# Optimization experiments

Hardware: AMD Instinct MI355X
Metric: run time of the kernel (lower is better)

The kernel has to match this reference:

```python
import jax, jax.numpy as jnp
import numpy as np

DIM = 128
HEADS = 4
KV_RANK = 64
Q_RANK = 32
ROPE = DIM // 2   # 64
NOPE = DIM // 2   # 64
VDIM = DIM // 2   # 64
B, H, W = 2, 64, 64
EPS = 1e-5


def _conv1x1(x, w, b):
    # x: [B,C,H,W], w: [O,C], b: [O]
    return jnp.einsum('bchw,oc->bohw', x, w) + b[None, :, None, None]


def _gn1(x, g, b):
    # GroupNorm with 1 group: normalize over (C,H,W) per sample
    mu = jnp.mean(x, axis=(1, 2, 3), keepdims=True)
    var = jnp.mean((x - mu) ** 2, axis=(1, 2, 3), keepdims=True)
    return (x - mu) / jnp.sqrt(var + EPS) * g[None, :, None, None] + b[None, :, None, None]


def _freqs(h, w):
    # Replicates RotaryPositionalEncoding: pe[...,0::4]=sin_h, 1::4=cos_h, 2::4=sin_w, 3::4=cos_w
    n = ROPE // 4
    inv = 1.0 / (10000.0 ** (jnp.arange(n, dtype=jnp.float32) / n))
    ah = jnp.arange(h, dtype=jnp.float32)[:, None] * inv  # [h,n]
    aw = jnp.arange(w, dtype=jnp.float32)[:, None] * inv  # [w,n]
    fh = jnp.stack([jnp.sin(ah), jnp.cos(ah)], -1)  # [h,n,2] -> (real=sin_h, imag=cos_h)
    fw = jnp.stack([jnp.sin(aw), jnp.cos(aw)], -1)  # [w,n,2]
    fh_b = jnp.broadcast_to(fh[:, None], (h, w, n, 2))
    fw_b = jnp.broadcast_to(fw[None, :], (h, w, n, 2))
    # interleave pairs: pair 2m -> fh[m], pair 2m+1 -> fw[m]
    pe = jnp.stack([fh_b, fw_b], axis=3).reshape(h * w, ROPE // 2, 2)
    return pe  # [S, ROPE//2, 2]


def _rope(x, f):
    # x: [..., S, ROPE]; f: [S, ROPE//2, 2]
    xp = x.reshape(x.shape[:-1] + (ROPE // 2, 2))
    fr, fi = f[..., 0], f[..., 1]  # [S, ROPE//2] broadcast over leading dims
    rr = xp[..., 0] * fr - xp[..., 1] * fi
    ri = xp[..., 0] * fi + xp[..., 1] * fr
    return jnp.stack([rr, ri], -1).reshape(x.shape)


def setup_inputs() -> dict:
    key = jax.random.key(0)
    ks = jax.random.split(key, 8)
    s = 0.02
    inp = {
        'x': jax.random.normal(ks[0], (B, DIM, H, W), dtype=jnp.float32),
        'q1_w': jax.random.normal(ks[1], (Q_RANK, DIM), dtype=jnp.float32) * s,
        'q1_b': jnp.zeros((Q_RANK,), jnp.float32),
        'q_gn_g': jnp.ones((Q_RANK,), jnp.float32),
        'q_gn_b': jnp.zeros((Q_RANK,), jnp.float32),
        'q2_w': jax.random.normal(ks[2], (HEADS * (NOPE + ROPE), Q_RANK), dtype=jnp.float32) * s,
        'q2_b': jnp.zeros((HEADS * (NOPE + ROPE),), jnp.float32),
        'kv1_w': jax.random.normal(ks[3], (KV_RANK + ROPE, DIM), dtype=jnp.float32) * s,
        'kv1_b': jnp.zeros((KV_RANK + ROPE,), jnp.float32),
        'kv_gn_g': jnp.ones((KV_RANK + ROPE,), jnp.float32),
        'kv_gn_b': jnp.zeros((KV_RANK + ROPE,), jnp.float32),
        'kvn_g': jnp.ones((KV_RANK,), jnp.float32),
        'kvn_b': jnp.zeros((KV_RANK,), jnp.float32),
        'kvup_w': jax.random.normal(ks[4], (HEADS * (NOPE + VDIM), KV_RANK), dtype=jnp.float32) * s,
        'kvup_b': jnp.zeros((HEADS * (NOPE + VDIM),), jnp.float32),
        'out_w': jax.random.normal(ks[5], (DIM, HEADS * VDIM), dtype=jnp.float32) * s,
        'out_b': jnp.zeros((DIM,), jnp.float32),
    }
    return inp


def reference(x, q1_w, q1_b, q_gn_g, q_gn_b, q2_w, q2_b, kv1_w, kv1_b, kv_gn_g, kv_gn_b, kvn_g, kvn_b, kvup_w, kvup_b, out_w, out_b):
    b, c, h, w = x.shape
    s = h * w
    f = _freqs(h, w)  # [S, ROPE//2, 2]

    # Q path: low-rank down -> GN -> up
    q = _conv1x1(_gn1(_conv1x1(x, q1_w, q1_b), q_gn_g, q_gn_b), q2_w, q2_b)
    q = q.reshape(b, HEADS, NOPE + ROPE, s).transpose(0, 1, 3, 2)  # [B,H,S,D]
    q_nope, q_rope = q[..., :NOPE], q[..., NOPE:]
    q = jnp.concatenate([q_nope, _rope(q_rope, f)], axis=-1)

    # KV path: joint down-proj, split rope-k and compressed kv
    kv = _gn1(_conv1x1(x, kv1_w, kv1_b), kv_gn_g, kv_gn_b)  # [B, ROPE+KV_RANK, H, W]
    k_rope_c, kv_c = kv[:, :ROPE], kv[:, ROPE:]
    kv_u = _conv1x1(_gn1(kv_c, kvn_g, kvn_b), kvup_w, kvup_b)
    kv_u = kv_u.reshape(b, HEADS, NOPE + VDIM, s).transpose(0, 1, 3, 2)
    k_nope, v = kv_u[..., :NOPE], kv_u[..., NOPE:]

    k_rope = _rope(k_rope_c.reshape(b, ROPE, s).transpose(0, 2, 1)[:, None], f)  # [B,1,S,ROPE]
    k = jnp.concatenate([k_nope, jnp.broadcast_to(k_rope, (b, HEADS, s, ROPE))], axis=-1)

    scale = (NOPE + ROPE) ** -0.5
    attn = jax.nn.softmax(jnp.einsum('bhqd,bhkd->bhqk', q, k) * scale, axis=-1)
    o = jnp.einsum('bhqk,bhkd->bhqd', attn, v)  # [B,H,S,VDIM]
    o = o.transpose(0, 1, 3, 2).reshape(b, HEADS * VDIM, h, w)
    return _conv1x1(o, out_w, out_b) + x
```

## Files before the change

### kernel.cpp

```cpp
#include <hip/hip_runtime.h>

typedef unsigned short ushort_t;
typedef unsigned int uint_t;
typedef __attribute__((ext_vector_type(8))) short s16x8;
typedef __attribute__((ext_vector_type(4))) short s16x4;
typedef __attribute__((ext_vector_type(4))) float f32x4;
typedef __attribute__((ext_vector_type(16))) float f32x16;

#define S_TOT 4096
#define QSCALE 0.08838834764831845f
#define LOG2E 1.4426950408889634f
#define QSL (QSCALE * LOG2E)
#define L2_10000_D16 0.8304820237218406f

__device__ __forceinline__ ushort_t f2b(float f) {
  uint_t u = __float_as_uint(f);
  uint_t r = (u + 0x7FFFu + ((u >> 16) & 1u)) >> 16;
  return (ushort_t)r;
}

__device__ __forceinline__ float b2f(ushort_t u) {
  return __uint_as_float((uint_t)u << 16);
}

__device__ __forceinline__ uint_t cvt_pk_bf16(float lo, float hi) {
  uint_t r;
  asm("v_cvt_pk_bf16_f32 %0, %1, %2" : "=v"(r) : "v"(lo), "v"(hi));
  return r;
}

__device__ __forceinline__ void gload16(const void* g, void* l) {
  __builtin_amdgcn_global_load_lds(
      (const __attribute__((address_space(1))) unsigned int*)g,
      (__attribute__((address_space(3))) unsigned int*)l, 16, 0, 0);
}

__device__ __forceinline__ void rope_pair_t(float& x0, float& x1, int p, int hi, int wi,
                                            float scale, const float2* __restrict__ tab) {
  int j = p >> 1;
  int src = (p & 1) ? wi : hi;
  float2 sc = tab[src * 16 + j];
  float r0 = (x0 * sc.x - x1 * sc.y) * scale;
  float r1 = (x0 * sc.y + x1 * sc.x) * scale;
  x0 = r0; x1 = r1;
}

__global__ __launch_bounds__(256) void k_conv1(
    const float* __restrict__ x, const float* __restrict__ q1_w, const float* __restrict__ q1_b,
    const float* __restrict__ kv1_w, const float* __restrict__ kv1_b,
    float* __restrict__ y_q, float* __restrict__ y_kv,
    const float* __restrict__ q2_w, const float* __restrict__ q2_b,
    const float* __restrict__ kvup_w, const float* __restrict__ kvup_b,
    const float* __restrict__ out_w, const float* __restrict__ out_b,
    ushort_t* __restrict__ wq2, ushort_t* __restrict__ wout,
    float* __restrict__ q2b2, float* __restrict__ outb2) {
  if (blockIdx.x >= 256) {
    int E = (blockIdx.x - 256) * 256 + threadIdx.x;
    if (E < 16384) {
      int oc = E >> 5, r = E & 31;
      int h = oc >> 7, d = oc & 127;
      float val;
      if (d < 64) {
        val = 0.f;
        for (int dd = 0; dd < 64; dd++)
          val += kvup_w[(h * 128 + dd) * 64 + d] * q2_w[(size_t)(h * 128 + dd) * 32 + r];
      } else {
        val = q2_w[(size_t)oc * 32 + r];
      }
      wq2[(size_t)oc * 32 + r] = f2b(val);
    } else if (E < 49152) {
      int e = E - 16384;
      int c = e >> 8, col = e & 255;
      int h = col >> 6, l = col & 63;
      float val = 0.f;
      for (int vd = 0; vd < 64; vd++)
        val += out_w[(size_t)c * 256 + h * 64 + vd] * kvup_w[(h * 128 + 64 + vd) * 64 + l];
      wout[(size_t)c * 256 + col] = f2b(val);
    } else if (E < 49664) {
      int oc = E - 49152;
      int h = oc >> 7, d = oc & 127;
      float val;
      if (d < 64) {
        val = 0.f;
        for (int dd = 0; dd < 64; dd++)
          val += kvup_w[(h * 128 + dd) * 64 + d] * q2_b[h * 128 + dd];
      } else val = q2_b[oc];
      q2b2[oc] = val;
    } else if (E < 49792) {
      int c = E - 49664;
      float val = out_b[c];
      for (int j = 0; j < 256; j++) {
        int h = j >> 6, vd = j & 63;
        val += out_w[(size_t)c * 256 + j] * kvup_b[h * 128 + 64 + vd];
      }
      outb2[c] = val;
    }
    return;
  }
  const int id = blockIdx.x;
  const int b = id >> 7, blk = id & 127, st = blk * 32;
  const int t = threadIdx.x, wid = t >> 6;
  const int l15 = t & 15, lg = (t >> 4) & 3;
  __shared__ __align__(16) ushort_t Xt[32][128];
  {
    const int si = t & 31, g = t >> 5;
#pragma unroll
    for (int half = 0; half < 2; half++) {
      ushort_t pk[8];
#pragma unroll
      for (int j = 0; j < 8; j++) {
        int c = g * 16 + half * 8 + j;
        pk[j] = f2b(x[(size_t)(b * 128 + c) * S_TOT + st + si]);
      }
      *(s16x8*)((char*)&Xt[si][0] + ((g * 32 + half * 16) ^ ((si & 15) << 4))) = *(s16x8*)pk;
    }
  }
  __syncthreads();
#pragma unroll
  for (int k5 = 0; k5 < 5; k5++) {
    const int tt = wid * 5 + k5;
    const int rt = tt >> 1, ct = tt & 1;
    const int oc0 = rt * 16;
    f32x4 acc;
#pragma unroll
    for (int r = 0; r < 4; r++) {
      int oc = oc0 + lg * 4 + r;
      acc[r] = (oc < 32) ? q1_b[oc] : kv1_b[oc - 32];
    }
    const int wrow = oc0 + l15;
    const float4* wr4 = (wrow < 32) ? ((const float4*)q1_w) + (size_t)wrow * 32
                                    : ((const float4*)kv1_w) + (size_t)(wrow - 32) * 32;
    const int xrow = ct * 16 + l15;
    const int xswz = (xrow & 15) << 4;
#pragma unroll
    for (int kk = 0; kk < 4; kk++) {
      float4 wa = wr4[kk * 8 + lg * 2];
      float4 wb = wr4[kk * 8 + lg * 2 + 1];
      ushort_t wp[8];
      wp[0] = f2b(wa.x); wp[1] = f2b(wa.y); wp[2] = f2b(wa.z); wp[3] = f2b(wa.w);
      wp[4] = f2b(wb.x); wp[5] = f2b(wb.y); wp[6] = f2b(wb.z); wp[7] = f2b(wb.w);
      s16x8 wf = *(s16x8*)wp;
      s16x8 xf = *(const s16x8*)((const char*)&Xt[xrow][0] + ((kk * 64 + lg * 16) ^ xswz));
      acc = __builtin_amdgcn_mfma_f32_16x16x32_bf16(wf, xf, acc, 0, 0, 0);
    }
    const int sp = st + ct * 16 + l15;
#pragma unroll
    for (int r = 0; r < 4; r++) {
      int oc = oc0 + lg * 4 + r;
      if (oc < 32) y_q[(size_t)(b * 32 + oc) * S_TOT + sp] = acc[r];
      else         y_kv[(size_t)(b * 128 + oc - 32) * S_TOT + sp] = acc[r];
    }
  }
}

__global__ __launch_bounds__(256) void k_red(
    const float* __restrict__ y_q, const float* __restrict__ y_kv,
    double* __restrict__ SQ) {
  const int pair = blockIdx.x, tid = threadIdx.x;
  const int lane = tid & 63, wid = tid >> 6;
  const int b = pair / 160, c = pair % 160;
  const float* row = (c < 32) ? y_q + ((size_t)(b * 32 + c) << 12)
                              : y_kv + ((size_t)(b * 128 + c - 32) << 12);
  const float4* r4 = (const float4*)row;
  double s = 0, q = 0;
#pragma unroll
  for (int j = 0; j < 4; j++) {
    float4 v = r4[tid * 4 + j];
    s += (double)v.x + (double)v.y + (double)v.z + (double)v.w;
    q += (double)v.x * v.x + (double)v.y * v.y + (double)v.z * v.z + (double)v.w * v.w;
  }
#pragma unroll
  for (int o = 1; o < 64; o <<= 1) { s += __shfl_xor(s, o, 64); q += __shfl_xor(q, o, 64); }
  __shared__ double red[4][2];
  if (lane == 0) { red[wid][0] = s; red[wid][1] = q; }
  __syncthreads();
  if (tid == 0) {
    SQ[pair * 2]     = red[0][0] + red[1][0] + red[2][0] + red[3][0];
    SQ[pair * 2 + 1] = red[0][1] + red[1][1] + red[2][1] + red[3][1];
  }
}

__global__ __launch_bounds__(512) void k_stats(
    const double* __restrict__ SQ,
    const float* __restrict__ qg, const float* __restrict__ qb,
    const float* __restrict__ kvg, const float* __restrict__ kvb,
    const float* __restrict__ kng, const float* __restrict__ knb,
    float* __restrict__ coef, float2* __restrict__ tab) {
  __shared__ double Sh[2][160], Qh[2][160];
  const int tid = threadIdx.x;
  for (int i = tid; i < 1024; i += 512) {
    int src = i >> 4, j = i & 15;
    float inv = exp2f(-(float)j * L2_10000_D16);
    float ang = (float)src * inv;
    tab[i] = make_float2(sinf(ang), cosf(ang));
  }
  if (tid < 320) {
    int b = tid / 160, c = tid % 160;
    Sh[b][c] = SQ[tid * 2]; Qh[b][c] = SQ[tid * 2 + 1];
  }
  __syncthreads();
  if (tid < 2) {
    int b = tid;
    float* cf = coef + b * 320;
    const double NS = 4096.0;
    double muq = 0, m2q = 0;
    for (int c = 0; c < 32; c++) { muq += Sh[b][c]; m2q += Qh[b][c]; }
    muq /= (32.0 * NS); m2q /= (32.0 * NS);
    double rstdq = 1.0 / sqrt(m2q - muq * muq + 1e-5);
    for (int c = 0; c < 32; c++) {
      double A = rstdq * (double)qg[c];
      cf[c] = (float)A; cf[32 + c] = (float)((double)qb[c] - muq * A);
    }
    double mukv = 0, m2kv = 0;
    for (int c = 0; c < 128; c++) { mukv += Sh[b][32 + c]; m2kv += Qh[b][32 + c]; }
    mukv /= (128.0 * NS); m2kv /= (128.0 * NS);
    double rstdkv = 1.0 / sqrt(m2kv - mukv * mukv + 1e-5);
    for (int c = 0; c < 64; c++) {
      double A = rstdkv * (double)kvg[c];
      cf[64 + c] = (float)A; cf[128 + c] = (float)((double)kvb[c] - mukv * A);
    }
    double mu2 = 0, m22 = 0;
    for (int c2 = 0; c2 < 64; c2++) {
      int c = 64 + c2;
      double a = rstdkv * (double)kvg[c], bb = (double)kvb[c] - mukv * a;
      double Ec = Sh[b][32 + c] / NS, M2c = Qh[b][32 + c] / NS;
      mu2 += a * Ec + bb;
      m22 += a * a * M2c + 2.0 * a * bb * Ec + bb * bb;
    }
    mu2 /= 64.0; m22 /= 64.0;
    double rstd2 = 1.0 / sqrt(m22 - mu2 * mu2 + 1e-5);
    for (int c2 = 0; c2 < 64; c2++) {
      int c = 64 + c2;
      double a = rstdkv * (double)kvg[c], bb = (double)kvb[c] - mukv * a;
      cf[192 + c2] = (float)(a * rstd2 * (double)kng[c2]);
      cf[256 + c2] = (float)((bb - mu2) * rstd2 * (double)kng[c2] + (double)knb[c2]);
    }
  }
}

__device__ __forceinline__ void gq_body(
    int id, ushort_t* smem,
    const float* __restrict__ y_q, const float* __restrict__ coef,
    const ushort_t* __restrict__ wq2, const float* __restrict__ q2b2,
    const float2* __restrict__ tab, ushort_t* __restrict__ Q) {
  const int h = id & 3, st = (id >> 2) & 63, b = id >> 8;
  const int t = threadIdx.x, si = t & 63, wid = t >> 6;
  const int l15 = t & 15, lg = (t >> 4) & 3;
  const float* cf = coef + b * 320;
  ushort_t* Xt = smem;
  ushort_t* sQ = smem + 4096;
  {
    ushort_t pk[8];
#pragma unroll
    for (int j = 0; j < 8; j++) {
      int c = wid * 8 + j;
      float v = y_q[(size_t)(b * 32 + c) * S_TOT + st * 64 + si];
      pk[j] = f2b(v * cf[c] + cf[32 + c]);
    }
    *(s16x8*)((char*)(Xt + si * 64) + ((wid * 16) ^ ((si & 7) << 4))) = *(s16x8*)pk;
  }
  __syncthreads();
  const int d0w = wid * 32;
  f32x4 acc[2][4];
#pragma unroll
  for (int db = 0; db < 2; db++) {
    f32x4 bv;
#pragma unroll
    for (int r = 0; r < 4; r++) bv[r] = q2b2[h * 128 + d0w + db * 16 + lg * 4 + r];
#pragma unroll
    for (int sb = 0; sb < 4; sb++) acc[db][sb] = bv;
  }
  s16x8 wf[2];
#pragma unroll
  for (int db = 0; db < 2; db++)
    wf[db] = *(const s16x8*)(wq2 + (size_t)(h * 128 + d0w + db * 16 + l15) * 32 + lg * 8);
  const int xsw = (lg * 16) ^ ((l15 & 7) << 4);
#pragma unroll
  for (int sb = 0; sb < 4; sb++) {
    s16x8 xf = *(const s16x8*)((const char*)(Xt + (sb * 16 + l15) * 64) + xsw);
#pragma unroll
    for (int db = 0; db < 2; db++)
      acc[db][sb] = __builtin_amdgcn_mfma_f32_16x16x32_bf16(wf[db], xf, acc[db][sb], 0, 0, 0);
  }
  if (wid >= 2) {
#pragma unroll
    for (int db = 0; db < 2; db++)
#pragma unroll
      for (int sb = 0; sb < 4; sb++) {
        int sp = st * 64 + sb * 16 + l15, hi = sp >> 6, wi = sp & 63;
        int dg = d0w + db * 16 + lg * 4;
#pragma unroll
        for (int pr = 0; pr < 2; pr++) {
          float v0 = acc[db][sb][pr * 2], v1 = acc[db][sb][pr * 2 + 1];
          int p = (dg + pr * 2 - 64) >> 1;
          rope_pair_t(v0, v1, p, hi, wi, QSL, tab);
          acc[db][sb][pr * 2] = v0; acc[db][sb][pr * 2 + 1] = v1;
        }
      }
  } else {
#pragma unroll
    for (int db = 0; db < 2; db++)
#pragma unroll
      for (int sb = 0; sb < 4; sb++)
#pragma unroll
        for (int r = 0; r < 4; r++) acc[db][sb][r] *= QSL;
  }
#pragma unroll
  for (int db = 0; db < 2; db++)
#pragma unroll
    for (int sb = 0; sb < 4; sb++) {
      ushort_t pk[4];
#pragma unroll
      for (int r = 0; r < 4; r++) pk[r] = f2b(acc[db][sb][r]);
      int srow = sb * 16 + l15;
      *(s16x4*)((char*)(sQ + srow * 128) + (((d0w + db * 16 + lg * 4) * 2) ^ ((srow & 7) << 4))) =
          *(s16x4*)pk;
    }
  __syncthreads();
  ushort_t* qrow = Q + ((size_t)(b * 4 + h) * S_TOT + st * 64 + si) * 128 + wid * 32;
#pragma unroll
  for (int j = 0; j < 4; j++) {
    s16x8 v = *(const s16x8*)((const char*)(sQ + si * 128) + ((wid * 64 + j * 16) ^ ((si & 7) << 4)));
    *(s16x8*)(qrow + j * 8) = v;
  }
}

__device__ __forceinline__ void lat_body(
    int blk, const float* __restrict__ y_kv, const float* __restrict__ coef,
    const float2* __restrict__ tab, ushort_t* __restrict__ C, ushort_t* __restrict__ VT) {
  const int b = blk >> 6, st = (blk & 63) * 64;
  const int t = threadIdx.x, si = t & 63, g = t >> 6;
  const float* cf = coef + b * 320;
  const int sp = st + si;
  if (g < 2) {
    const int c0 = g * 32;
    float v[32];
#pragma unroll
    for (int j = 0; j < 32; j++) {
      int c = c0 + j;
      v[j] = y_kv[(size_t)(b * 128 + c) * S_TOT + sp] * cf[64 + c] + cf[128 + c];
    }
    const int hi = sp >> 6, wi = sp & 63;
#pragma unroll
    for (int k = 0; k < 16; k++)
      rope_pair_t(v[2 * k], v[2 * k + 1], (c0 >> 1) + k, hi, wi, 1.0f, tab);
    ushort_t pk[32];
#pragma unroll
    for (int j = 0; j < 32; j++) pk[j] = f2b(v[j]);
    ushort_t* crow = C + (size_t)(b * S_TOT + sp) * 128 + 64 + c0;
#pragma unroll
    for (int j4 = 0; j4 < 4; j4++) *(s16x8*)(crow + j4 * 8) = *(s16x8*)(pk + j4 * 8);
  } else {
    const int c0 = (g - 2) * 32;
    ushort_t pk[32];
#pragma unroll
    for (int j = 0; j < 32; j++) {
      int c2 = c0 + j;
      float v = y_kv[(size_t)(b * 128 + 64 + c2) * S_TOT + sp] * cf[192 + c2] + cf[256 + c2];
      ushort_t u = f2b(v);
      pk[j] = u;
      VT[(size_t)(b * 64 + c2) * S_TOT + sp] = u;
    }
    ushort_t* crow = C + (size_t)(b * S_TOT + sp) * 128 + c0;
#pragma unroll
    for (int j4 = 0; j4 < 4; j4++) *(s16x8*)(crow + j4 * 8) = *(s16x8*)(pk + j4 * 8);
  }
}

__global__ __launch_bounds__(256) void k_build(
    const float* __restrict__ y_q, const float* __restrict__ y_kv,
    const float* __restrict__ coef,
    const ushort_t* __restrict__ wq2, const float* __restrict__ q2b2,
    const float2* __restrict__ tab,
    ushort_t* __restrict__ Q, ushort_t* __restrict__ C, ushort_t* __restrict__ VT) {
  __shared__ __align__(16) ushort_t smem[12288];
  if (blockIdx.x < 512) gq_body(blockIdx.x, smem, y_q, coef, wq2, q2b2, tab, Q);
  else                  lat_body(blockIdx.x - 512, y_kv, coef, tab, C, VT);
}

__global__ __launch_bounds__(256, 2) void k_attn(
    const ushort_t* __restrict__ Q, const ushort_t* __restrict__ C,
    const ushort_t* __restrict__ VT, ushort_t* __restrict__ Opart,
    float* __restrict__ lvec) {
  const int bid = blockIdx.x;
  const int bh = bid & 7;
  const int rest = bid >> 3;
  const int half = rest >> 5, qblk = rest & 31;
  const int kv0 = half * 2048;
  const int tid = threadIdx.x;
  const int wid = tid >> 6, lane = tid & 63;
  const int l31 = lane & 31, hi = lane >> 5;
  const int qbase = qblk * 128 + wid * 32;
  const int b4 = bh >> 2;
  const ushort_t* Qp = Q + (size_t)bh * S_TOT * 128;
  const ushort_t* Kp = C + (size_t)b4 * S_TOT * 128;
  const ushort_t* Vp = VT + (size_t)b4 * 64 * S_TOT;

  __shared__ __align__(16) ushort_t K_lds[3][64][128];
  __shared__ __align__(16) ushort_t V_lds[3][64][64];

  s16x8 qf[8];
#pragma unroll
  for (int c = 0; c < 8; c++)
    qf[c] = *(const s16x8*)(Qp + (size_t)(qbase + l31) * 128 + c * 16 + hi * 8);

  f32x16 o0, o1;
#pragma unroll
  for (int r = 0; r < 16; r++) { o0[r] = 0.f; o1[r] = 0.f; }
  float l_s = 0.f;

  const int krow_l = tid >> 4;
  const int kcolb = (tid & 15) * 16;
  const int vrow_l = tid >> 3;
  const int vcolb = (tid & 7) * 16;

#define STAGE(kvb, bufi)                                                          \
  {                                                                               \
    _Pragma("unroll")                                                             \
    for (int i = 0; i < 4; i++) {                                                 \
      int row = i * 16 + krow_l;                                                  \
      int colb = kcolb ^ ((row & 15) << 4);                                       \
      gload16((const char*)(Kp + (size_t)((kvb) + row) * 128) + colb,             \
              (void*)&K_lds[bufi][i * 16 + wid * 4][0]);                          \
    }                                                                             \
    _Pragma("unroll")                                                             \
    for (int i = 0; i < 2; i++) {                                                 \
      int vd = i * 32 + vrow_l;                                                   \
      int colb = vcolb ^ ((vd & 7) << 4);                                         \
      gload16((const char*)(Vp + (size_t)vd * S_TOT + (kvb)) + colb,              \
              (void*)&V_lds[bufi][i * 32 + wid * 8][0]);                          \
    }                                                                             \
  }

  STAGE(kv0, 0);
  STAGE(kv0 + 64, 1);

  const int kswz = (l31 & 15) << 4;
  const int vswz = (l31 & 7) << 4;
#pragma unroll 1
  for (int t = 0; t < 32; t++) {
    const int buf = t % 3;
    if (t < 31) {
      asm volatile("s_waitcnt vmcnt(6)" ::: "memory");
    } else {
      asm volatile("s_waitcnt vmcnt(0)" ::: "memory");
    }
    __builtin_amdgcn_sched_barrier(0);
    __builtin_amdgcn_s_barrier();
    __builtin_amdgcn_sched_barrier(0);
    if (t < 30) STAGE(kv0 + (t + 2) * 64, (t + 2) % 3);
    f32x16 sc0, sc1;
#pragma unroll
    for (int r = 0; r < 16; r++) { sc0[r] = 0.f; sc1[r] = 0.f; }
    __builtin_amdgcn_s_setprio(1);
#pragma unroll
    for (int c = 0; c < 8; c++) {
      const int off = (c * 32 + hi * 16) ^ kswz;
      s16x8 k0 = *(const s16x8*)((const char*)&K_lds[buf][l31][0] + off);
      s16x8 k1 = *(const s16x8*)((const char*)&K_lds[buf][32 + l31][0] + off);
      sc0 = __builtin_amdgcn_mfma_f32_32x32x16_bf16(k0, qf[c], sc0, 0, 0, 0);
      sc1 = __builtin_amdgcn_mfma_f32_32x32x16_bf16(k1, qf[c], sc1, 0, 0, 0);
    }
    __builtin_amdgcn_s_setprio(0);
    float rs = 0.f;
#pragma unroll
    for (int r = 0; r < 16; r++) {
      float p0 = exp2f(sc0[r]);
      float p1 = exp2f(sc1[r]);
      sc0[r] = p0; sc1[r] = p1;
      rs += p0 + p1;
    }
    l_s += rs;
    __builtin_amdgcn_s_setprio(1);
#pragma unroll
    for (int c = 0; c < 4; c++) {
      const f32x16 P = (c < 2) ? sc0 : sc1;
      const int rA = 8 * (c & 1);
      uint_t a0 = cvt_pk_bf16(P[rA + 0], P[rA + 1]);
      uint_t a1 = cvt_pk_bf16(P[rA + 2], P[rA + 3]);
      uint_t b0 = cvt_pk_bf16(P[rA + 4], P[rA + 5]);
      uint_t b1 = cvt_pk_bf16(P[rA + 6], P[rA + 7]);
      asm volatile("v_permlane32_swap_b32 %0, %1" : "+v"(a0), "+v"(b0));
      asm volatile("v_permlane32_swap_b32 %0, %1" : "+v"(a1), "+v"(b1));
      union { uint_t u[4]; s16x8 v; } pf;
      pf.u[0] = a0; pf.u[1] = a1;
      pf.u[2] = b0; pf.u[3] = b1;
      const int voff = (c * 32 + hi * 16) ^ vswz;
      s16x8 v0 = *(const s16x8*)((const char*)&V_lds[buf][l31][0] + voff);
      s16x8 v1 = *(const s16x8*)((const char*)&V_lds[buf][32 + l31][0] + voff);
      o0 = __builtin_amdgcn_mfma_f32_32x32x16_bf16(v0, pf.v, o0, 0, 0, 0);
      o1 = __builtin_amdgcn_mfma_f32_32x32x16_bf16(v1, pf.v, o1, 0, 0, 0);
    }
    __builtin_amdgcn_s_setprio(0);
  }
#undef STAGE
  l_s += __shfl_xor(l_s, 32, 64);
  if (lane < 32)
    lvec[((size_t)(half * 8 + bh) << 12) + qbase + l31] = l_s;
  char* sO = (char*)&K_lds[0][0][0];
#pragma unroll
  for (int vt = 0; vt < 2; vt++) {
#pragma unroll
    for (int r = 0; r < 16; r += 2) {
      float v0 = (vt ? o1[r] : o0[r]);
      float v1 = (vt ? o1[r + 1] : o0[r + 1]);
      uint_t u = cvt_pk_bf16(v0, v1);
      int vd = vt * 32 + (r & 3) + 8 * (r >> 2) + 4 * hi;
      *(uint_t*)(sO + (wid * 32 + l31) * 128 + ((vd * 2) ^ ((l31 & 7) << 4))) = u;
    }
  }
  __syncthreads();
  {
    const int r = tid >> 1, hf = tid & 1;
    const int w = r >> 5, ql = r & 31;
    ushort_t* orow = Opart + ((size_t)(half * 8 + bh) * S_TOT + qblk * 128 + r) * 64 + hf * 32;
#pragma unroll
    for (int j = 0; j < 4; j++) {
      s16x8 v = *(const s16x8*)(sO + (w * 32 + ql) * 128 + ((hf * 64 + j * 16) ^ ((ql & 7) << 4)));
      *(s16x8*)(orow + j * 8) = v;
    }
  }
}

__global__ __launch_bounds__(256) void k_oc(
    const ushort_t* __restrict__ Opart, const float* __restrict__ lvec,
    const ushort_t* __restrict__ wout, const float* __restrict__ outb2,
    const float* __restrict__ x, float* __restrict__ out) {
  const int id = blockIdx.x;
  const int cch = id & 1, st32 = (id >> 1) & 127, b = id >> 8;
  const int t = threadIdx.x, wid = t >> 6;
  const int l15 = t & 15, lg = (t >> 4) & 3;
  __shared__ __align__(16) ushort_t Xt[32][256];
  {
    const int s = t & 31, grp = t >> 5;
    const int h = grp >> 1, vd0 = (grp & 1) * 32;
    const int sp = st32 * 32 + s;
    const float l0 = lvec[((size_t)(b * 4 + h) << 12) + sp];
    const float l1 = lvec[((size_t)(8 + b * 4 + h) << 12) + sp];
    const float w = 1.f / (l0 + l1);
    const ushort_t* oa = Opart + ((size_t)(b * 4 + h) * S_TOT + sp) * 64 + vd0;
    const ushort_t* obp = oa + (size_t)8 * S_TOT * 64;
#pragma unroll
    for (int j4 = 0; j4 < 4; j4++) {
      union { s16x8 v; ushort_t u[8]; } av, bv2;
      av.v = *(const s16x8*)(oa + j4 * 8);
      bv2.v = *(const s16x8*)(obp + j4 * 8);
      ushort_t pk[8];
#pragma unroll
      for (int j = 0; j < 8; j++) pk[j] = f2b(w * (b2f(av.u[j]) + b2f(bv2.u[j])));
      *(s16x8*)((char*)&Xt[s][0] + ((grp * 64 + j4 * 16) ^ ((s & 7) << 4))) = *(s16x8*)pk;
    }
  }
  __syncthreads();
  const int c0w = cch * 64 + wid * 16;
  f32x4 acc[2];
  {
    f32x4 bv;
#pragma unroll
    for (int r = 0; r < 4; r++) bv[r] = outb2[c0w + lg * 4 + r];
    acc[0] = bv; acc[1] = bv;
  }
#pragma unroll
  for (int kk = 0; kk < 8; kk++) {
    s16x8 wf = *(const s16x8*)(wout + (size_t)(c0w + l15) * 256 + kk * 32 + lg * 8);
#pragma unroll
    for (int sb = 0; sb < 2; sb++) {
      s16x8 xf = *(const s16x8*)((const char*)&Xt[sb * 16 + l15][0] +
                                 ((kk * 64 + lg * 16) ^ ((l15 & 7) << 4)));
      acc[sb] = __builtin_amdgcn_mfma_f32_16x16x32_bf16(wf, xf, acc[sb], 0, 0, 0);
    }
  }
#pragma unroll
  for (int sb = 0; sb < 2; sb++) {
#pragma unroll
    for (int r = 0; r < 4; r++) {
      int c = c0w + lg * 4 + r;
      int sp = st32 * 32 + sb * 16 + l15;
      size_t idx = (size_t)(b * 128 + c) * S_TOT + sp;
      out[idx] = acc[sb][r] + x[idx];
    }
  }
}

extern "C" void kernel_launch(void* const* d_in, const int* in_sizes, int n_in,
                              void* d_out, int out_size, void* d_ws, size_t ws_size,
                              hipStream_t stream) {
  const float* x      = (const float*)d_in[0];
  const float* q1_w   = (const float*)d_in[1];
  const float* q1_b   = (const float*)d_in[2];
  const float* q_gn_g = (const float*)d_in[3];
  const float* q_gn_b = (const float*)d_in[4];
  const float* q2_w   = (const float*)d_in[5];
  const float* q2_b   = (const float*)d_in[6];
  const float* kv1_w  = (const float*)d_in[7];
  const float* kv1_b  = (const float*)d_in[8];
  const float* kv_gn_g= (const float*)d_in[9];
  const float* kv_gn_b= (const float*)d_in[10];
  const float* kvn_g  = (const float*)d_in[11];
  const float* kvn_b  = (const float*)d_in[12];
  const float* kvup_w = (const float*)d_in[13];
  const float* kvup_b = (const float*)d_in[14];
  const float* out_w  = (const float*)d_in[15];
  const float* out_b  = (const float*)d_in[16];

  const size_t MB = 1u << 20;
  char* ws = (char*)d_ws;
  float*    y_q   = (float*)(ws);
  float*    y_kv  = (float*)(ws + 1 * MB);
  ushort_t* Q     = (ushort_t*)(ws + 5 * MB);
  ushort_t* C     = (ushort_t*)(ws + 13 * MB);
  ushort_t* VT    = (ushort_t*)(ws + 15 * MB);
  double*   SQ    = (double*)(ws + 19 * MB);
  float*    coef  = (float*)(ws + 19 * MB + 8192);
  ushort_t* wq2   = (ushort_t*)(ws + 19 * MB + 16384);
  ushort_t* wout  = (ushort_t*)(ws + 19 * MB + 65536);
  float*    q2b2  = (float*)(ws + 19 * MB + 131072);
  float*    outb2 = (float*)(ws + 19 * MB + 139264);
  float2*   tab   = (float2*)(ws + 19 * MB + 143360);
  ushort_t* Opart = (ushort_t*)(ws + 20 * MB);
  float*    lvec  = (float*)(ws + 28 * MB);
  float*    out   = (float*)d_out;

  k_conv1<<<451, 256, 0, stream>>>(x, q1_w, q1_b, kv1_w, kv1_b, y_q, y_kv,
                                   q2_w, q2_b, kvup_w, kvup_b, out_w, out_b,
                                   wq2, wout, q2b2, outb2);
  k_red  <<<320, 256, 0, stream>>>(y_q, y_kv, SQ);
  k_stats<<<1,   512, 0, stream>>>(SQ, q_gn_g, q_gn_b, kv_gn_g, kv_gn_b, kvn_g, kvn_b,
                                   coef, tab);
  k_build<<<640, 256, 0, stream>>>(y_q, y_kv, coef, wq2, q2b2, tab, Q, C, VT);
  k_attn <<<512, 256, 0, stream>>>(Q, C, VT, Opart, lvec);
  k_oc   <<<512, 256, 0, stream>>>(Opart, lvec, wout, outb2, x, out);
}
```

Measured before the change: 126.2 us.

## Fuse Q up-projection and RoPE into attention kernel prologue

The Q low-rank up-projection, GroupNorm affine, scaling and RoPE now run inside the attention kernel. Each block builds its own 128-row Q tile with 32x32x16 MFMAs and uses permlane32 swaps to put the result straight into the Q fragment layout. This removes the bf16 Q tensor written to and read back from global memory, and k_build shrinks to a latent-only k_lat kernel. In exchange, the Q tile is recomputed once per KV half, the attention prologue gets longer, and k_lat launches only 128 blocks.

```diff
diff --git a/kernel.cpp b/kernel.cpp
--- a/kernel.cpp
+++ b/kernel.cpp
@@ -238,96 +238,10 @@
   }
 }
 
-__device__ __forceinline__ void gq_body(
-    int id, ushort_t* smem,
-    const float* __restrict__ y_q, const float* __restrict__ coef,
-    const ushort_t* __restrict__ wq2, const float* __restrict__ q2b2,
-    const float2* __restrict__ tab, ushort_t* __restrict__ Q) {
-  const int h = id & 3, st = (id >> 2) & 63, b = id >> 8;
-  const int t = threadIdx.x, si = t & 63, wid = t >> 6;
-  const int l15 = t & 15, lg = (t >> 4) & 3;
-  const float* cf = coef + b * 320;
-  ushort_t* Xt = smem;
-  ushort_t* sQ = smem + 4096;
-  {
-    ushort_t pk[8];
-#pragma unroll
-    for (int j = 0; j < 8; j++) {
-      int c = wid * 8 + j;
-      float v = y_q[(size_t)(b * 32 + c) * S_TOT + st * 64 + si];
-      pk[j] = f2b(v * cf[c] + cf[32 + c]);
-    }
-    *(s16x8*)((char*)(Xt + si * 64) + ((wid * 16) ^ ((si & 7) << 4))) = *(s16x8*)pk;
-  }
-  __syncthreads();
-  const int d0w = wid * 32;
-  f32x4 acc[2][4];
-#pragma unroll
-  for (int db = 0; db < 2; db++) {
-    f32x4 bv;
-#pragma unroll
-    for (int r = 0; r < 4; r++) bv[r] = q2b2[h * 128 + d0w + db * 16 + lg * 4 + r];
-#pragma unroll
-    for (int sb = 0; sb < 4; sb++) acc[db][sb] = bv;
-  }
-  s16x8 wf[2];
-#pragma unroll
-  for (int db = 0; db < 2; db++)
-    wf[db] = *(const s16x8*)(wq2 + (size_t)(h * 128 + d0w + db * 16 + l15) * 32 + lg * 8);
-  const int xsw = (lg * 16) ^ ((l15 & 7) << 4);
-#pragma unroll
-  for (int sb = 0; sb < 4; sb++) {
-    s16x8 xf = *(const s16x8*)((const char*)(Xt + (sb * 16 + l15) * 64) + xsw);
-#pragma unroll
-    for (int db = 0; db < 2; db++)
-      acc[db][sb] = __builtin_amdgcn_mfma_f32_16x16x32_bf16(wf[db], xf, acc[db][sb], 0, 0, 0);
-  }
-  if (wid >= 2) {
-#pragma unroll
-    for (int db = 0; db < 2; db++)
-#pragma unroll
-      for (int sb = 0; sb < 4; sb++) {
-        int sp = st * 64 + sb * 16 + l15, hi = sp >> 6, wi = sp & 63;
-        int dg = d0w + db * 16 + lg * 4;
-#pragma unroll
-        for (int pr = 0; pr < 2; pr++) {
-          float v0 = acc[db][sb][pr * 2], v1 = acc[db][sb][pr * 2 + 1];
-          int p = (dg + pr * 2 - 64) >> 1;
-          rope_pair_t(v0, v1, p, hi, wi, QSL, tab);
-          acc[db][sb][pr * 2] = v0; acc[db][sb][pr * 2 + 1] = v1;
-        }
-      }
-  } else {
-#pragma unroll
-    for (int db = 0; db < 2; db++)
-#pragma unroll
-      for (int sb = 0; sb < 4; sb++)
-#pragma unroll
-        for (int r = 0; r < 4; r++) acc[db][sb][r] *= QSL;
-  }
-#pragma unroll
-  for (int db = 0; db < 2; db++)
-#pragma unroll
-    for (int sb = 0; sb < 4; sb++) {
-      ushort_t pk[4];
-#pragma unroll
-      for (int r = 0; r < 4; r++) pk[r] = f2b(acc[db][sb][r]);
-      int srow = sb * 16 + l15;
-      *(s16x4*)((char*)(sQ + srow * 128) + (((d0w + db * 16 + lg * 4) * 2) ^ ((srow & 7) << 4))) =
-          *(s16x4*)pk;
-    }
-  __syncthreads();
-  ushort_t* qrow = Q + ((size_t)(b * 4 + h) * S_TOT + st * 64 + si) * 128 + wid * 32;
-#pragma unroll
-  for (int j = 0; j < 4; j++) {
-    s16x8 v = *(const s16x8*)((const char*)(sQ + si * 128) + ((wid * 64 + j * 16) ^ ((si & 7) << 4)));
-    *(s16x8*)(qrow + j * 8) = v;
-  }
-}
-
-__device__ __forceinline__ void lat_body(
-    int blk, const float* __restrict__ y_kv, const float* __restrict__ coef,
+__global__ __launch_bounds__(256) void k_lat(
+    const float* __restrict__ y_kv, const float* __restrict__ coef,
     const float2* __restrict__ tab, ushort_t* __restrict__ C, ushort_t* __restrict__ VT) {
+  const int blk = blockIdx.x;
   const int b = blk >> 6, st = (blk & 63) * 64;
   const int t = threadIdx.x, si = t & 63, g = t >> 6;
   const float* cf = coef + b * 320;
@@ -367,21 +281,12 @@
   }
 }
 
-__global__ __launch_bounds__(256) void k_build(
-    const float* __restrict__ y_q, const float* __restrict__ y_kv,
-    const float* __restrict__ coef,
+__global__ __launch_bounds__(256, 2) void k_attn(
+    const float* __restrict__ y_q, const float* __restrict__ coef,
     const ushort_t* __restrict__ wq2, const float* __restrict__ q2b2,
     const float2* __restrict__ tab,
-    ushort_t* __restrict__ Q, ushort_t* __restrict__ C, ushort_t* __restrict__ VT) {
-  __shared__ __align__(16) ushort_t smem[12288];
-  if (blockIdx.x < 512) gq_body(blockIdx.x, smem, y_q, coef, wq2, q2b2, tab, Q);
-  else                  lat_body(blockIdx.x - 512, y_kv, coef, tab, C, VT);
-}
-
-__global__ __launch_bounds__(256, 2) void k_attn(
-    const ushort_t* __restrict__ Q, const ushort_t* __restrict__ C,
-    const ushort_t* __restrict__ VT, ushort_t* __restrict__ Opart,
-    float* __restrict__ lvec) {
+    const ushort_t* __restrict__ C, const ushort_t* __restrict__ VT,
+    ushort_t* __restrict__ Opart, float* __restrict__ lvec) {
   const int bid = blockIdx.x;
   const int bh = bid & 7;
   const int rest = bid >> 3;
@@ -392,7 +297,6 @@
   const int l31 = lane & 31, hi = lane >> 5;
   const int qbase = qblk * 128 + wid * 32;
   const int b4 = bh >> 2;
-  const ushort_t* Qp = Q + (size_t)bh * S_TOT * 128;
   const ushort_t* Kp = C + (size_t)b4 * S_TOT * 128;
   const ushort_t* Vp = VT + (size_t)b4 * 64 * S_TOT;
 
@@ -400,9 +304,63 @@
   __shared__ __align__(16) ushort_t V_lds[3][64][64];
 
   s16x8 qf[8];
-#pragma unroll
-  for (int c = 0; c < 8; c++)
-    qf[c] = *(const s16x8*)(Qp + (size_t)(qbase + l31) * 128 + c * 16 + hi * 8);
+  {
+    ushort_t* Xq = (ushort_t*)&K_lds[0][0][0];
+    const float* cf = coef + b4 * 320;
+    {
+      const int si = tid & 127, g = tid >> 7;
+      ushort_t pk[16];
+#pragma unroll
+      for (int j = 0; j < 16; j++) {
+        int c = g * 16 + j;
+        float v = y_q[(size_t)(b4 * 32 + c) * S_TOT + qblk * 128 + si];
+        pk[j] = f2b(v * cf[c] + cf[32 + c]);
+      }
+      *(s16x8*)((char*)(Xq + si * 64) + ((g * 32) ^ ((si & 7) << 4))) = *(s16x8*)pk;
+      *(s16x8*)((char*)(Xq + si * 64) + ((g * 32 + 16) ^ ((si & 7) << 4))) = *(s16x8*)(pk + 8);
+    }
+    __syncthreads();
+    const int h = bh & 3;
+    const int qrow = wid * 32 + l31;
+    const int qsw = (qrow & 7) << 4;
+    const int sp = qbase + l31, hip = sp >> 6, wip = sp & 63;
+#pragma unroll
+    for (int tq = 0; tq < 4; tq++) {
+      f32x16 dq;
+#pragma unroll
+      for (int r = 0; r < 16; r++)
+        dq[r] = q2b2[h * 128 + 32 * tq + (r & 3) + 8 * (r >> 2) + 4 * hi];
+#pragma unroll
+      for (int kk = 0; kk < 2; kk++) {
+        s16x8 wf = *(const s16x8*)(wq2 + (size_t)(h * 128 + tq * 32 + l31) * 32 + kk * 16 + hi * 8);
+        s16x8 xf = *(const s16x8*)((const char*)(Xq + qrow * 64) + ((kk * 32 + hi * 16) ^ qsw));
+        dq = __builtin_amdgcn_mfma_f32_32x32x16_bf16(wf, xf, dq, 0, 0, 0);
+      }
+#pragma unroll
+      for (int m = 0; m < 8; m++) {
+        const int r = 2 * m;
+        const int dg = 32 * tq + (r & 3) + 8 * (r >> 2) + 4 * hi;
+        float v0 = dq[r], v1 = dq[r + 1];
+        if (tq >= 2) rope_pair_t(v0, v1, (dg - 64) >> 1, hip, wip, QSL, tab);
+        else { v0 *= QSL; v1 *= QSL; }
+        dq[r] = v0; dq[r + 1] = v1;
+      }
+#pragma unroll
+      for (int hc = 0; hc < 2; hc++) {
+        const int rA = 8 * hc;
+        uint_t a0 = cvt_pk_bf16(dq[rA + 0], dq[rA + 1]);
+        uint_t a1 = cvt_pk_bf16(dq[rA + 2], dq[rA + 3]);
+        uint_t b0 = cvt_pk_bf16(dq[rA + 4], dq[rA + 5]);
+        uint_t b1 = cvt_pk_bf16(dq[rA + 6], dq[rA + 7]);
+        asm volatile("v_permlane32_swap_b32 %0, %1" : "+v"(a0), "+v"(b0));
+        asm volatile("v_permlane32_swap_b32 %0, %1" : "+v"(a1), "+v"(b1));
+        union { uint_t u[4]; s16x8 v; } pfq;
+        pfq.u[0] = a0; pfq.u[1] = a1; pfq.u[2] = b0; pfq.u[3] = b1;
+        qf[2 * tq + hc] = pfq.v;
+      }
+    }
+    __syncthreads();
+  }
 
   f32x16 o0, o1;
 #pragma unroll
@@ -607,7 +565,6 @@
   char* ws = (char*)d_ws;
   float*    y_q   = (float*)(ws);
   float*    y_kv  = (float*)(ws + 1 * MB);
-  ushort_t* Q     = (ushort_t*)(ws + 5 * MB);
   ushort_t* C     = (ushort_t*)(ws + 13 * MB);
   ushort_t* VT    = (ushort_t*)(ws + 15 * MB);
   double*   SQ    = (double*)(ws + 19 * MB);
@@ -627,7 +584,7 @@
   k_red  <<<320, 256, 0, stream>>>(y_q, y_kv, SQ);
   k_stats<<<1,   512, 0, stream>>>(SQ, q_gn_g, q_gn_b, kv_gn_g, kv_gn_b, kvn_g, kvn_b,
                                    coef, tab);
-  k_build<<<640, 256, 0, stream>>>(y_q, y_kv, coef, wq2, q2b2, tab, Q, C, VT);
-  k_attn <<<512, 256, 0, stream>>>(Q, C, VT, Opart, lvec);
+  k_lat  <<<128, 256, 0, stream>>>(y_kv, coef, tab, C, VT);
+  k_attn <<<512, 256, 0, stream>>>(y_q, coef, wq2, q2b2, tab, C, VT, Opart, lvec);
   k_oc   <<<512, 256, 0, stream>>>(Opart, lvec, wout, outb2, x, out);
 }
```

Measured after the change: 124.5 us, median of 2. No clear change (-1.3%).
